# Kernel optimization log

Measured on AMD Instinct MI355X. Metric: run time of the kernel, lower is better.

The kernel has to match this reference:

```python
import jax, jax.numpy as jnp
import numpy as np

MAX_LABELS = 512  # labels 1..512, 0 = background

def setup_inputs() -> dict:
    key = jax.random.key(0)
    k1, k2, k3 = jax.random.split(key, 3)
    B, C, H, W = 4, 16, 1024, 1024
    pred = jax.random.normal(k1, (B, C, H, W), dtype=jnp.float32)
    target = jax.random.normal(k2, (B, C, H, W), dtype=jnp.float32)
    nuclei = jax.random.randint(k3, (B, 1, H, W), 0, MAX_LABELS + 1, dtype=jnp.int32)
    return {"pred": pred, "target": target, "nuclei": nuclei}

def reference(pred, target, nuclei):
    # scale_factor == 1.0 -> no interpolation branch.
    B, C, H, W = pred.shape
    num_seg = MAX_LABELS + 1  # per-image segments, slot 0 = background
    labels = nuclei.reshape(B, H * W)                          # [B, HW] int
    ids = (labels + jnp.arange(B, dtype=labels.dtype)[:, None] * num_seg).reshape(-1)
    pf = pred.transpose(0, 2, 3, 1).reshape(-1, C)             # [B*HW, C]
    tf = target.transpose(0, 2, 3, 1).reshape(-1, C)
    pred_sums = jax.ops.segment_sum(pf, ids, num_segments=B * num_seg)
    target_sums = jax.ops.segment_sum(tf, ids, num_segments=B * num_seg)
    counts = jax.ops.segment_sum(jnp.ones_like(ids, dtype=pred.dtype), ids,
                                 num_segments=B * num_seg)
    # drop background slot, reshape to [B, MAX_LABELS, C]
    pred_sums = pred_sums.reshape(B, num_seg, C)[:, 1:]
    target_sums = target_sums.reshape(B, num_seg, C)[:, 1:]
    counts = counts.reshape(B, num_seg)[:, 1:]                 # [B, MAX_LABELS]
    denom = jnp.maximum(counts, 1.0)[..., None]
    pred_means = (pred_sums / denom).reshape(B * MAX_LABELS, C)
    target_means = (target_sums / denom).reshape(B * MAX_LABELS, C)
    label_range = jnp.arange(1, MAX_LABELS + 1, dtype=nuclei.dtype)
    cell_ids = jnp.where(counts > 0, label_range[None, :], 0).reshape(-1)
    return pred_means, target_means, cell_ids
```

## Files before the change

kernel.cpp:

```cpp
#include <hip/hip_runtime.h>

#define B_IMG 4
#define CCH 16
#define HW (1024 * 1024)
#define SEG 513
#define PADU 17
#define THREADS 512
#define BLOCKS_PER_IMG 128
#define GRID (B_IMG * BLOCKS_PER_IMG)
#define PIX_PER_BLOCK (HW / BLOCKS_PER_IMG)
#define QUADS (PIX_PER_BLOCK / (THREADS * 4))

#define FXSCALE 8192.0f
#define FXINV   (1.0f / 8192.0f)
#define FXBIAS  131072

#define WS_PRED 0
#define WS_TGT  (B_IMG * SEG * CCH)
#define WS_CNT  (2 * B_IMG * SEG * CCH)
#define WS_FLOATS (WS_CNT + B_IMG * SEG)

#define OUT_TGT  (B_IMG * 512 * CCH)
#define OUT_CELL (2 * B_IMG * 512 * CCH)

__device__ __forceinline__ unsigned long long pack2(float p, float t) {
    unsigned int ip = (unsigned int)(__float2int_rn(p * FXSCALE) + FXBIAS);
    unsigned int it = (unsigned int)(__float2int_rn(t * FXSCALE) + FXBIAS);
    return (unsigned long long)ip | ((unsigned long long)it << 32);
}

__global__ __launch_bounds__(THREADS, 2)
void accum_kernel(const float* __restrict__ pred,
                  const float* __restrict__ target,
                  const int* __restrict__ nuclei,
                  float* __restrict__ ws) {
    __shared__ unsigned long long s_acc[SEG * PADU];
    __shared__ unsigned int s_cnt[SEG];

    const int tid = threadIdx.x;
    for (int i = tid; i < SEG * PADU; i += THREADS) s_acc[i] = 0ull;
    for (int i = tid; i < SEG; i += THREADS) s_cnt[i] = 0u;
    __syncthreads();

    const int b   = blockIdx.x / BLOCKS_PER_IMG;
    const int blk = blockIdx.x % BLOCKS_PER_IMG;

    const int*   nuc = nuclei + b * HW + blk * PIX_PER_BLOCK;
    const float* pr  = pred   + b * CCH * HW + blk * PIX_PER_BLOCK;
    const float* tg  = target + b * CCH * HW + blk * PIX_PER_BLOCK;

    for (int q = 0; q < QUADS; ++q) {
        const int p = (q * THREADS + tid) * 4;
        const int4 lab = *(const int4*)(nuc + p);

        unsigned long long* a0 = &s_acc[lab.x * PADU];
        unsigned long long* a1 = &s_acc[lab.y * PADU];
        unsigned long long* a2 = &s_acc[lab.z * PADU];
        unsigned long long* a3 = &s_acc[lab.w * PADU];

        atomicAdd(&s_cnt[lab.x], 1u);
        atomicAdd(&s_cnt[lab.y], 1u);
        atomicAdd(&s_cnt[lab.z], 1u);
        atomicAdd(&s_cnt[lab.w], 1u);

#pragma unroll
        for (int c = 0; c < CCH; ++c) {
            const float4 pv = *(const float4*)(pr + c * HW + p);
            const float4 tv = *(const float4*)(tg + c * HW + p);
            atomicAdd(a0 + c, pack2(pv.x, tv.x));
            atomicAdd(a1 + c, pack2(pv.y, tv.y));
            atomicAdd(a2 + c, pack2(pv.z, tv.z));
            atomicAdd(a3 + c, pack2(pv.w, tv.w));
        }
    }
    __syncthreads();

    float* ws_pred = ws + WS_PRED + b * SEG * CCH;
    float* ws_tgt  = ws + WS_TGT  + b * SEG * CCH;
    float* ws_cnt  = ws + WS_CNT  + b * SEG;
    for (int i = tid; i < SEG * CCH; i += THREADS) {
        const int sg = i >> 4, c = i & 15;
        const unsigned long long v = s_acc[sg * PADU + c];
        const long long bias = (long long)s_cnt[sg] * (long long)FXBIAS;
        const long long lo = (long long)(v & 0xffffffffull) - bias;
        const long long hi = (long long)(v >> 32) - bias;
        unsafeAtomicAdd(&ws_pred[i], (float)lo * FXINV);
        unsafeAtomicAdd(&ws_tgt[i],  (float)hi * FXINV);
    }
    for (int i = tid; i < SEG; i += THREADS) {
        unsafeAtomicAdd(&ws_cnt[i], (float)s_cnt[i]);
    }
}

__global__ void finalize_kernel(const float* __restrict__ ws, float* __restrict__ out) {
    const int t = blockIdx.x * blockDim.x + threadIdx.x;
    if (t >= B_IMG * 512) return;
    const int b = t >> 9;
    const int l = (t & 511) + 1;

    const float cnt   = ws[WS_CNT + b * SEG + l];
    const float denom = fmaxf(cnt, 1.f);

    const float* sp = ws + WS_PRED + (b * SEG + l) * CCH;
    const float* st = ws + WS_TGT  + (b * SEG + l) * CCH;
#pragma unroll
    for (int c = 0; c < CCH; ++c) {
        out[t * CCH + c]           = sp[c] / denom;
        out[OUT_TGT + t * CCH + c] = st[c] / denom;
    }
    out[OUT_CELL + t] = (cnt > 0.f) ? (float)l : 0.f;
}

extern "C" void kernel_launch(void* const* d_in, const int* in_sizes, int n_in,
                              void* d_out, int out_size, void* d_ws, size_t ws_size,
                              hipStream_t stream) {
    const float* pred   = (const float*)d_in[0];
    const float* target = (const float*)d_in[1];
    const int*   nuclei = (const int*)d_in[2];
    float* out = (float*)d_out;
    float* ws  = (float*)d_ws;

    hipMemsetAsync(d_ws, 0, WS_FLOATS * sizeof(float), stream);
    accum_kernel<<<GRID, THREADS, 0, stream>>>(pred, target, nuclei, ws);
    finalize_kernel<<<8, 256, 0, stream>>>(ws, out);
}
```

Baseline: 530.0 us.

## Split channels across two blocks to shrink LDS and raise occupancy

Each pixel range is now handled by two blocks, each covering 8 of the 16 channels. This halves the per-block shared-memory accumulator so more blocks fit per CU, and the launch bound is raised to match. Loads become nontemporal. The fixed-point bias is now subtracted in the finalize kernel in float rather than per block, which removes integer work from the epilogue but costs some float precision on large biased sums. Label reads are duplicated across the two channel halves.

Result: no change. 536.2 us (+1.2%).

```diff
diff --git a/kernel.cpp b/kernel.cpp
--- a/kernel.cpp
+++ b/kernel.cpp
@@ -2,18 +2,19 @@
 
 #define B_IMG 4
 #define CCH 16
+#define HALF_C 8
 #define HW (1024 * 1024)
 #define SEG 513
-#define PADU 17
+#define PADU 9
 #define THREADS 512
 #define BLOCKS_PER_IMG 128
-#define GRID (B_IMG * BLOCKS_PER_IMG)
+#define GRID (B_IMG * BLOCKS_PER_IMG * 2)
 #define PIX_PER_BLOCK (HW / BLOCKS_PER_IMG)
 #define QUADS (PIX_PER_BLOCK / (THREADS * 4))
 
 #define FXSCALE 8192.0f
 #define FXINV   (1.0f / 8192.0f)
-#define FXBIAS  131072
+#define FXBIAS  131072.0f
 
 #define WS_PRED 0
 #define WS_TGT  (B_IMG * SEG * CCH)
@@ -23,13 +24,15 @@
 #define OUT_TGT  (B_IMG * 512 * CCH)
 #define OUT_CELL (2 * B_IMG * 512 * CCH)
 
+typedef float v4f __attribute__((ext_vector_type(4)));
+
 __device__ __forceinline__ unsigned long long pack2(float p, float t) {
-    unsigned int ip = (unsigned int)(__float2int_rn(p * FXSCALE) + FXBIAS);
-    unsigned int it = (unsigned int)(__float2int_rn(t * FXSCALE) + FXBIAS);
+    unsigned int ip = (unsigned int)(__float2int_rn(p * FXSCALE) + 131072);
+    unsigned int it = (unsigned int)(__float2int_rn(t * FXSCALE) + 131072);
     return (unsigned long long)ip | ((unsigned long long)it << 32);
 }
 
-__global__ __launch_bounds__(THREADS, 2)
+__global__ __launch_bounds__(THREADS, 8)
 void accum_kernel(const float* __restrict__ pred,
                   const float* __restrict__ target,
                   const int* __restrict__ nuclei,
@@ -42,12 +45,16 @@
     for (int i = tid; i < SEG; i += THREADS) s_cnt[i] = 0u;
     __syncthreads();
 
-    const int b   = blockIdx.x / BLOCKS_PER_IMG;
-    const int blk = blockIdx.x % BLOCKS_PER_IMG;
+    const int gb  = blockIdx.x;
+    const int h   = gb & 1;
+    const int rb  = gb >> 1;
+    const int b   = rb / BLOCKS_PER_IMG;
+    const int blk = rb % BLOCKS_PER_IMG;
+    const int c0  = h * HALF_C;
 
     const int*   nuc = nuclei + b * HW + blk * PIX_PER_BLOCK;
-    const float* pr  = pred   + b * CCH * HW + blk * PIX_PER_BLOCK;
-    const float* tg  = target + b * CCH * HW + blk * PIX_PER_BLOCK;
+    const float* pr  = pred   + (size_t)(b * CCH + c0) * HW + blk * PIX_PER_BLOCK;
+    const float* tg  = target + (size_t)(b * CCH + c0) * HW + blk * PIX_PER_BLOCK;
 
     for (int q = 0; q < QUADS; ++q) {
         const int p = (q * THREADS + tid) * 4;
@@ -58,15 +65,17 @@
         unsigned long long* a2 = &s_acc[lab.z * PADU];
         unsigned long long* a3 = &s_acc[lab.w * PADU];
 
-        atomicAdd(&s_cnt[lab.x], 1u);
-        atomicAdd(&s_cnt[lab.y], 1u);
-        atomicAdd(&s_cnt[lab.z], 1u);
-        atomicAdd(&s_cnt[lab.w], 1u);
+        if (h == 0) {
+            atomicAdd(&s_cnt[lab.x], 1u);
+            atomicAdd(&s_cnt[lab.y], 1u);
+            atomicAdd(&s_cnt[lab.z], 1u);
+            atomicAdd(&s_cnt[lab.w], 1u);
+        }
 
 #pragma unroll
-        for (int c = 0; c < CCH; ++c) {
-            const float4 pv = *(const float4*)(pr + c * HW + p);
-            const float4 tv = *(const float4*)(tg + c * HW + p);
+        for (int c = 0; c < HALF_C; ++c) {
+            const v4f pv = __builtin_nontemporal_load((const v4f*)(pr + c * HW + p));
+            const v4f tv = __builtin_nontemporal_load((const v4f*)(tg + c * HW + p));
             atomicAdd(a0 + c, pack2(pv.x, tv.x));
             atomicAdd(a1 + c, pack2(pv.y, tv.y));
             atomicAdd(a2 + c, pack2(pv.z, tv.z));
@@ -78,17 +87,18 @@
     float* ws_pred = ws + WS_PRED + b * SEG * CCH;
     float* ws_tgt  = ws + WS_TGT  + b * SEG * CCH;
     float* ws_cnt  = ws + WS_CNT  + b * SEG;
-    for (int i = tid; i < SEG * CCH; i += THREADS) {
-        const int sg = i >> 4, c = i & 15;
-        const unsigned long long v = s_acc[sg * PADU + c];
-        const long long bias = (long long)s_cnt[sg] * (long long)FXBIAS;
-        const long long lo = (long long)(v & 0xffffffffull) - bias;
-        const long long hi = (long long)(v >> 32) - bias;
-        unsafeAtomicAdd(&ws_pred[i], (float)lo * FXINV);
-        unsafeAtomicAdd(&ws_tgt[i],  (float)hi * FXINV);
+    for (int i = tid; i < SEG * HALF_C; i += THREADS) {
+        const int sg = i >> 3, cc = i & 7;
+        const unsigned long long v = s_acc[sg * PADU + cc];
+        const unsigned int lo = (unsigned int)(v & 0xffffffffull);
+        const unsigned int hi = (unsigned int)(v >> 32);
+        unsafeAtomicAdd(&ws_pred[sg * CCH + c0 + cc], (float)lo);
+        unsafeAtomicAdd(&ws_tgt[sg * CCH + c0 + cc],  (float)hi);
     }
-    for (int i = tid; i < SEG; i += THREADS) {
-        unsafeAtomicAdd(&ws_cnt[i], (float)s_cnt[i]);
+    if (h == 0) {
+        for (int i = tid; i < SEG; i += THREADS) {
+            unsafeAtomicAdd(&ws_cnt[i], (float)s_cnt[i]);
+        }
     }
 }
 
@@ -100,13 +110,14 @@
 
     const float cnt   = ws[WS_CNT + b * SEG + l];
     const float denom = fmaxf(cnt, 1.f);
+    const float bias  = cnt * FXBIAS;
 
     const float* sp = ws + WS_PRED + (b * SEG + l) * CCH;
     const float* st = ws + WS_TGT  + (b * SEG + l) * CCH;
 #pragma unroll
     for (int c = 0; c < CCH; ++c) {
-        out[t * CCH + c]           = sp[c] / denom;
-        out[OUT_TGT + t * CCH + c] = st[c] / denom;
+        out[t * CCH + c]           = (sp[c] - bias) * FXINV / denom;
+        out[OUT_TGT + t * CCH + c] = (st[c] - bias) * FXINV / denom;
     }
     out[OUT_CELL + t] = (cnt > 0.f) ? (float)l : 0.f;
 }
```
